# Kernel tuning notes

Measured on AMD Instinct MI355X. Metric: run time of the kernel, lower is better.

## Reference

```python
import jax, jax.numpy as jnp
import numpy as np
from jax import lax

DN = ('NCDHW', 'OIDHW', 'NCDHW')
BN_EPS = 1e-5  # eval-mode BatchNorm3d with running_mean=0, running_var=1


def conv3d(x, w, b):
    y = lax.conv_general_dilated(x, w, window_strides=(1, 1, 1),
                                 padding=[(1, 1)] * 3, dimension_numbers=DN)
    return y + b[None, :, None, None, None]


def maxpool2(x):
    return lax.reduce_window(x, -jnp.inf, lax.max,
                             (1, 1, 2, 2, 2), (1, 1, 2, 2, 2), 'VALID')


def spline_block(x, cw, cb, knots, sw, w1, w2, g, beta):
    # SplineConv3d: conv -> (BSpline3D blend with SiLU) -> BN(eval) -> maxpool
    y = conv3d(x, cw, cb)                                   # [b,c,d,h,w]
    basis = jnp.maximum(y[..., None] - knots, 0.0) ** 3     # [b,c,d,h,w,k]
    sp = jnp.einsum('bcdhwk,ck->bcdhw', basis, sw)
    out = (w1[None, :, None, None, None] * sp
           + w2[None, :, None, None, None] * (y * jax.nn.sigmoid(y)))
    scale = (g / jnp.sqrt(1.0 + BN_EPS))[None, :, None, None, None]
    return maxpool2(out * scale + beta[None, :, None, None, None])


def setup_inputs() -> dict:
    key = jax.random.key(0)
    ks = iter(jax.random.split(key, 40))
    def nrm(shape, s=1.0):
        return jax.random.normal(next(ks), shape, dtype=jnp.float32) * s
    d = {}
    d['x'] = nrm((2, 1, 64, 64, 64))
    for cin, cout, t in [(1, 32, '1'), (32, 64, '2'), (64, 128, '3')]:
        d[f'c{t}_w'] = nrm((cout, cin, 3, 3, 3), 0.1)
        d[f'c{t}_b'] = nrm((cout,), 0.01)
        d[f'c{t}_knots'] = jnp.linspace(-1.0, 1.0, 10).astype(jnp.float32)
        d[f'c{t}_sw'] = nrm((cout, 10), 0.2)
        d[f'c{t}_w1'] = nrm((cout,), 0.2)
        d[f'c{t}_w2'] = nrm((cout,), 0.2)
        d[f'bn{t}_g'] = 1.0 + nrm((cout,), 0.1)
        d[f'bn{t}_b'] = nrm((cout,), 0.1)
    d['fc1_w'] = nrm((256, 128), 0.05)
    d['fc1_b'] = nrm((256,), 0.01)
    d['fc2_w'] = nrm((2, 256), 0.05)
    d['fc2_b'] = nrm((2,), 0.01)
    return d


def reference(x,
              c1_w, c1_b, c1_knots, c1_sw, c1_w1, c1_w2, bn1_g, bn1_b,
              c2_w, c2_b, c2_knots, c2_sw, c2_w1, c2_w2, bn2_g, bn2_b,
              c3_w, c3_b, c3_knots, c3_sw, c3_w1, c3_w2, bn3_g, bn3_b,
              fc1_w, fc1_b, fc2_w, fc2_b):
    h = spline_block(x, c1_w, c1_b, c1_knots, c1_sw, c1_w1, c1_w2, bn1_g, bn1_b)
    h = spline_block(h, c2_w, c2_b, c2_knots, c2_sw, c2_w1, c2_w2, bn2_g, bn2_b)
    h = spline_block(h, c3_w, c3_b, c3_knots, c3_sw, c3_w1, c3_w2, bn3_g, bn3_b)
    h = h.mean(axis=(2, 3, 4))          # AdaptiveAvgPool3d((1,1,1)) + flatten
    h = jax.nn.relu(h @ fc1_w.T + fc1_b)  # dropout is identity in eval mode
    return h @ fc2_w.T + fc2_b
```

## Files before the change

kernel.cpp:

```cpp
#include <hip/hip_runtime.h>
#include <math.h>


#define GLOBAL_AS __attribute__((address_space(1)))
#define LDS_AS    __attribute__((address_space(3)))

static __device__ __forceinline__ void async_ld16(const float* g, float* l) {
    __builtin_amdgcn_global_load_lds((const GLOBAL_AS void*)g, (LDS_AS void*)l,
                                     16, 0, 0);
}

template <int TPB_, int CIN, int CSPLIT, int G, int PDT, int PHT, int PWT, bool AL>
__global__ __launch_bounds__(TPB_, 2) void spline_block_kernel(
    const float* __restrict__ x,
    const float* __restrict__ cw,
    const float* __restrict__ cb,
    const float* __restrict__ knots,
    const float* __restrict__ sw,
    const float* __restrict__ w1,
    const float* __restrict__ w2,
    const float* __restrict__ g,
    const float* __restrict__ beta,
    const float* __restrict__ zbuf,
    float* __restrict__ out,
    int N, int Cout, int D, int H, int W, int WP,
    int OWP, int OWO,
    int ntiles, int nthw, int ntw)
{
    constexpr int SP     = PDT * PHT * PWT;
    constexpr int CPG    = CIN / CSPLIT;
    constexpr int ID     = 2 * PDT + 2;
    constexpr int IH     = 2 * PHT + 2;
    constexpr int CPR    = AL ? 5 : 6;
    constexpr int PITCH  = CPR * 4;
    constexpr int ROWS   = ID * IH;
    constexpr int CHUNKS = ROWS * CPR;
    constexpr int PHYS   = ROWS * PITCH;
    constexpr int NCH    = (CHUNKS + SP - 1) / SP;
    constexpr int BUFS   = (CPG > 1) ? 2 : 1;
    static_assert(SP * CSPLIT == TPB_, "block = CSPLIT x SP");
    static_assert(CIN % CSPLIT == 0, "cin divisible");
    static_assert(NCH <= 32, "mask fits u32");
    static_assert(!AL || (PWT % 8) == 0, "aligned path needs 16-dword tile step");
    static_assert(CSPLIT == 1 ||
                  (CSPLIT - 1) * SP * G * 8 <= CSPLIT * BUFS * PHYS,
                  "reduction scratch fits in tile");

    __shared__ __align__(16) float tile[CSPLIT][BUFS][PHYS];
    __shared__ float  wlds[CIN * G * 28];
    __shared__ float4 stbl[G * 11];

    const int PD = D >> 1, PH = H >> 1, PW = W >> 1;
    const int groups = Cout / G;
    const int tid  = threadIdx.x;
    const int cg   = tid / SP;
    const int stid = tid % SP;

    const int bx      = blockIdx.x;
    const int tile_id = bx % ntiles;
    const int t1      = bx / ntiles;
    const int grp     = t1 % groups;
    const int n       = t1 / groups;
    const int c0      = grp * G;
    const int cinbase = cg * CPG;

    const int td  = tile_id / nthw;
    const int rem = tile_id % nthw;
    const int th_ = rem / ntw;
    const int tw_ = rem % ntw;

    for (int i = tid; i < CIN * G * 27; i += TPB_) {
        const int t  = i % 27;
        const int cgr = i / 27;
        const int gg = cgr % G;
        const int ci = cgr / G;
        wlds[cgr * 28 + t] = cw[((c0 + gg) * CIN + ci) * 27 + t];
    }
    for (int i = tid; i < G * 11; i += TPB_) {
        const int gg  = i / 11;
        const int cnt = i % 11;
        const int c   = c0 + gg;
        float A = 0.f, B3 = 0.f, C3 = 0.f, Dd = 0.f;
        for (int j = 0; j < cnt; j++) {
            const float s = sw[c * 10 + j];
            const float k = knots[j];
            A  += s;
            B3 += 3.0f * s * k;
            C3 += 3.0f * s * k * k;
            Dd += s * k * k * k;
        }
        stbl[i] = make_float4(A, B3, C3, Dd);
    }

    const int pwl = stid % PWT;
    const int phl = (stid / PWT) % PHT;
    const int pdl = stid / (PWT * PHT);

    const int pd0 = td * PDT, ph0 = th_ * PHT, pw0 = tw_ * PWT;
    const int d0 = 2 * pd0 - 1, h0 = 2 * ph0 - 1;
    const int w0 = 2 * pw0 - 1;
    const int sorg  = AL ? (2 * pw0) : (w0 & ~3);
    const int woff  = AL ? 0 : (w0 - sorg);

    int off[NCH];
    unsigned vm = 0;
#pragma unroll
    for (int k = 0; k < NCH; k++) {
        const int chunk = stid + SP * k;
        const int row = chunk / CPR, cs = chunk - row * CPR;
        const int dz = row / IH, hy = row - dz * IH;
        const int dd = d0 + dz, hh = h0 + hy;
        const int wsd = sorg + cs * 4;
        bool ok = (chunk < CHUNKS) &
                  ((unsigned)dd < (unsigned)D) &
                  ((unsigned)hh < (unsigned)H);
        if (!AL) ok = ok & ((unsigned)wsd < (unsigned)W);
        off[k] = ok ? (dd * H + hh) * WP + wsd : 0;
        vm |= (unsigned)ok << k;
    }

    const size_t chstride = (size_t)D * H * WP;
    const float* xn = x + (size_t)n * CIN * chstride;

    float acc[G][8];
#pragma unroll
    for (int gg = 0; gg < G; gg++)
#pragma unroll
        for (int i = 0; i < 8; i++) acc[gg][i] = 0.0f;

    __syncthreads();

    {
        const float* xc = xn + (size_t)cinbase * chstride;
        float* dst = &tile[cg][0][0];
#pragma unroll
        for (int k = 0; k < NCH; k++) {
            const int chunk = stid + SP * k;
            if ((k + 1) * SP <= CHUNKS || chunk < CHUNKS) {
                const float* src = ((vm >> k) & 1) ? (xc + off[k]) : zbuf;
                async_ld16(src, dst + chunk * 4);
            }
        }
    }
    __syncthreads();

    int cur = 0;
#pragma unroll 1
    for (int s = 0; s < CPG; s++) {
        if (s + 1 < CPG) {
            const float* xc = xn + (size_t)(cinbase + s + 1) * chstride;
            float* dst = &tile[cg][cur ^ (BUFS - 1)][0];
#pragma unroll
            for (int k = 0; k < NCH; k++) {
                const int chunk = stid + SP * k;
                if ((k + 1) * SP <= CHUNKS || chunk < CHUNKS) {
                    const float* src = ((vm >> k) & 1) ? (xc + off[k]) : zbuf;
                    async_ld16(src, dst + chunk * 4);
                }
            }
        }

        const int ci = cinbase + s;
        const float* tb = &tile[cg][cur][0];
        float r[64];
#pragma unroll
        for (int dz = 0; dz < 4; dz++)
#pragma unroll
        for (int dy = 0; dy < 4; dy++) {
            const int rb = ((2 * pdl + dz) * IH + (2 * phl + dy)) * PITCH +
                           woff + 2 * pwl;
            if (AL) {
                const float2 v0 = *(const float2*)(tb + rb);
                const float2 v1 = *(const float2*)(tb + rb + 2);
                r[(dz * 4 + dy) * 4 + 0] = v0.x;
                r[(dz * 4 + dy) * 4 + 1] = v0.y;
                r[(dz * 4 + dy) * 4 + 2] = v1.x;
                r[(dz * 4 + dy) * 4 + 3] = v1.y;
            } else {
                r[(dz * 4 + dy) * 4 + 0] = tb[rb + 0];
                r[(dz * 4 + dy) * 4 + 1] = tb[rb + 1];
                r[(dz * 4 + dy) * 4 + 2] = tb[rb + 2];
                r[(dz * 4 + dy) * 4 + 3] = tb[rb + 3];
            }
        }

#pragma unroll
        for (int gg = 0; gg < G; gg++) {
            const float4* w4p = (const float4*)&wlds[(ci * G + gg) * 28];
#pragma unroll
            for (int ch = 0; ch < 7; ch++) {
                const float4 wv = w4p[ch];
#pragma unroll
                for (int j = 0; j < 4; j++) {
                    const int tap = ch * 4 + j;
                    if (tap < 27) {
                        const float wvj = (j == 0) ? wv.x : (j == 1) ? wv.y
                                        : (j == 2) ? wv.z : wv.w;
                        const int kd = tap / 9, kh = (tap % 9) / 3, kw = tap % 3;
#pragma unroll
                        for (int od = 0; od < 2; od++)
#pragma unroll
                        for (int oh = 0; oh < 2; oh++)
#pragma unroll
                        for (int ow = 0; ow < 2; ow++)
                            acc[gg][(od * 2 + oh) * 2 + ow] =
                                fmaf(wvj,
                                     r[((od + kd) * 4 + (oh + kh)) * 4 + (ow + kw)],
                                     acc[gg][(od * 2 + oh) * 2 + ow]);
                    }
                }
            }
        }

        if (s + 1 < CPG) {
            __syncthreads();
            cur ^= 1;
        }
    }

    float* af = &acc[0][0];
    if (CSPLIT > 1) {
        __syncthreads();
        float* scratch = &tile[0][0][0];
        if (cg > 0) {
#pragma unroll
            for (int idx = 0; idx < G * 8; idx++)
                scratch[(idx * (CSPLIT - 1) + (cg - 1)) * SP + stid] = af[idx];
        }
        __syncthreads();
        if (cg == 0) {
#pragma unroll
            for (int idx = 0; idx < G * 8; idx++) {
                float s = af[idx];
                for (int j = 0; j < CSPLIT - 1; j++)
                    s += scratch[(idx * (CSPLIT - 1) + j) * SP + stid];
                af[idx] = s;
            }
        }
    }

    if (cg == 0) {
        const int pdg = pd0 + pdl, phg = ph0 + phl, pwg = pw0 + pwl;
#pragma unroll
        for (int gg = 0; gg < G; gg++) {
            const int c = c0 + gg;
            const float bias = cb[c];
            const float W1 = w1[c], W2 = w2[c];
            const float scale = g[c] * rsqrtf(1.0f + 1e-5f);
            const float bb = beta[c];

            float m = -INFINITY;
#pragma unroll
            for (int i = 0; i < 8; i++) {
                const float y = acc[gg][i] + bias;
                int idx = (int)floorf((y + 1.0f) * 4.5f) + 1;
                idx = min(max(idx, 0), 10);
                const float4 cf = stbl[gg * 11 + idx];
                const float sp = ((cf.x * y - cf.y) * y + cf.z) * y - cf.w;
                const float silu = y / (1.0f + __expf(-y));
                const float o = fmaf(W1 * sp + W2 * silu, scale, bb);
                m = fmaxf(m, o);
            }
            out[(((size_t)(n * Cout + c) * PD + pdg) * PH + phg) * OWP + OWO + pwg]
                = m;
        }
    }
}

__global__ __launch_bounds__(64) void mean_kernel(
    const float* __restrict__ h, float* __restrict__ out, int S)
{
    const int nc = blockIdx.x;
    const int lane = threadIdx.x;
    const float* p = h + (size_t)nc * S;
    float s = 0.0f;
    for (int i = lane; i < S; i += 64) s += p[i];
#pragma unroll
    for (int off = 32; off > 0; off >>= 1) s += __shfl_down(s, off, 64);
    if (lane == 0) out[nc] = s / (float)S;
}

__global__ __launch_bounds__(256) void fc_kernel(
    const float* __restrict__ pooled,
    const float* __restrict__ w1, const float* __restrict__ b1,
    const float* __restrict__ w2, const float* __restrict__ b2,
    float* __restrict__ out)
{
    __shared__ float hbuf[2][256];
    const int j = threadIdx.x;
#pragma unroll
    for (int nn = 0; nn < 2; nn++) {
        float s = b1[j];
        for (int k = 0; k < 128; k++)
            s = fmaf(pooled[nn * 128 + k], w1[j * 128 + k], s);
        hbuf[nn][j] = fmaxf(s, 0.0f);
    }
    __syncthreads();
    const int wid = j >> 6, lane = j & 63;
    const int nn = wid >> 1, oo = wid & 1;
    float s = 0.0f;
    for (int k = lane; k < 256; k += 64) s += hbuf[nn][k] * w2[oo * 256 + k];
#pragma unroll
    for (int off = 32; off > 0; off >>= 1) s += __shfl_down(s, off, 64);
    if (lane == 0) out[nn * 2 + oo] = s + b2[oo];
}

extern "C" void kernel_launch(void* const* d_in, const int* in_sizes, int n_in,
                              void* d_out, int out_size, void* d_ws, size_t ws_size,
                              hipStream_t stream) {
    const float* x      = (const float*)d_in[0];
    const float* c1_w   = (const float*)d_in[1];
    const float* c1_b   = (const float*)d_in[2];
    const float* c1_kn  = (const float*)d_in[3];
    const float* c1_sw  = (const float*)d_in[4];
    const float* c1_w1  = (const float*)d_in[5];
    const float* c1_w2  = (const float*)d_in[6];
    const float* bn1_g  = (const float*)d_in[7];
    const float* bn1_b  = (const float*)d_in[8];
    const float* c2_w   = (const float*)d_in[9];
    const float* c2_b   = (const float*)d_in[10];
    const float* c2_kn  = (const float*)d_in[11];
    const float* c2_sw  = (const float*)d_in[12];
    const float* c2_w1  = (const float*)d_in[13];
    const float* c2_w2  = (const float*)d_in[14];
    const float* bn2_g  = (const float*)d_in[15];
    const float* bn2_b  = (const float*)d_in[16];
    const float* c3_w   = (const float*)d_in[17];
    const float* c3_b   = (const float*)d_in[18];
    const float* c3_kn  = (const float*)d_in[19];
    const float* c3_sw  = (const float*)d_in[20];
    const float* c3_w1  = (const float*)d_in[21];
    const float* c3_w2  = (const float*)d_in[22];
    const float* bn3_g  = (const float*)d_in[23];
    const float* bn3_b  = (const float*)d_in[24];
    const float* fc1_w  = (const float*)d_in[25];
    const float* fc1_b  = (const float*)d_in[26];
    const float* fc2_w  = (const float*)d_in[27];
    const float* fc2_b  = (const float*)d_in[28];

    float* ws = (float*)d_ws;
    float* h1     = ws;
    float* h2     = h1 + 2359296;
    float* h3     = h2 + 655360;
    float* pooled = h3 + 131072;
    float* zbuf   = pooled + 256;

    hipMemsetAsync(zbuf, 0, 64, stream);
    hipMemsetAsync(h1, 0, 2359296 * sizeof(float), stream);
    hipMemsetAsync(h2, 0, 655360 * sizeof(float), stream);

    spline_block_kernel<256, 1, 1, 4, 4, 8, 8, false>
        <<<dim3(2048), dim3(256), 0, stream>>>(
        x, c1_w, c1_b, c1_kn, c1_sw, c1_w1, c1_w2, bn1_g, bn1_b, zbuf, h1,
        2, 32, 64, 64, 64, 64, 36, 1, 128, 16, 4);
    spline_block_kernel<256, 32, 1, 4, 4, 8, 8, true>
        <<<dim3(512), dim3(256), 0, stream>>>(
        h1, c2_w, c2_b, c2_kn, c2_sw, c2_w1, c2_w2, bn2_g, bn2_b, zbuf, h2,
        2, 64, 32, 32, 32, 36, 20, 1, 16, 4, 2);
    spline_block_kernel<256, 64, 4, 4, 2, 4, 8, true>
        <<<dim3(512), dim3(256), 0, stream>>>(
        h2, c3_w, c3_b, c3_kn, c3_sw, c3_w1, c3_w2, bn3_g, bn3_b, zbuf, h3,
        2, 128, 16, 16, 16, 20, 8, 0, 8, 2, 1);
    mean_kernel<<<dim3(256), dim3(64), 0, stream>>>(h3, pooled, 512);
    fc_kernel<<<dim3(1), dim3(256), 0, stream>>>(pooled, fc1_w, fc1_b, fc2_w, fc2_b,
                                                 (float*)d_out);
}
```

Baseline: 342.6 us.

## Load conv weights as scalar loads instead of LDS and split cin for block 2

Removes the LDS weight staging array and instead loads each output channel's 27 taps through a wave-uniform (readfirstlane) pointer, so they can be served by scalar loads from cache, and the gg loop is no longer unrolled. Block 2 now splits its input channels across two thread groups over a smaller spatial tile, doubling the grid size. This is meant to cut LDS traffic and footprint and to raise parallelism. In exchange it adds scalar memory latency inside the inner loop and a cross-group reduction step.

```diff
diff --git a/kernel.cpp b/kernel.cpp
--- a/kernel.cpp
+++ b/kernel.cpp
@@ -47,7 +47,6 @@
                   "reduction scratch fits in tile");
 
     __shared__ __align__(16) float tile[CSPLIT][BUFS][PHYS];
-    __shared__ float  wlds[CIN * G * 28];
     __shared__ float4 stbl[G * 11];
 
     const int PD = D >> 1, PH = H >> 1, PW = W >> 1;
@@ -69,13 +68,6 @@
     const int th_ = rem / ntw;
     const int tw_ = rem % ntw;
 
-    for (int i = tid; i < CIN * G * 27; i += TPB_) {
-        const int t  = i % 27;
-        const int cgr = i / 27;
-        const int gg = cgr % G;
-        const int ci = cgr / G;
-        wlds[cgr * 28 + t] = cw[((c0 + gg) * CIN + ci) * 27 + t];
-    }
     for (int i = tid; i < G * 11; i += TPB_) {
         const int gg  = i / 11;
         const int cnt = i % 11;
@@ -184,31 +176,31 @@
             }
         }
 
-#pragma unroll
+#pragma unroll 1
         for (int gg = 0; gg < G; gg++) {
-            const float4* w4p = (const float4*)&wlds[(ci * G + gg) * 28];
-#pragma unroll
-            for (int ch = 0; ch < 7; ch++) {
-                const float4 wv = w4p[ch];
-#pragma unroll
-                for (int j = 0; j < 4; j++) {
-                    const int tap = ch * 4 + j;
-                    if (tap < 27) {
-                        const float wvj = (j == 0) ? wv.x : (j == 1) ? wv.y
-                                        : (j == 2) ? wv.z : wv.w;
-                        const int kd = tap / 9, kh = (tap % 9) / 3, kw = tap % 3;
-#pragma unroll
-                        for (int od = 0; od < 2; od++)
-#pragma unroll
-                        for (int oh = 0; oh < 2; oh++)
-#pragma unroll
-                        for (int ow = 0; ow < 2; ow++)
-                            acc[gg][(od * 2 + oh) * 2 + ow] =
-                                fmaf(wvj,
-                                     r[((od + kd) * 4 + (oh + kh)) * 4 + (ow + kw)],
-                                     acc[gg][(od * 2 + oh) * 2 + ow]);
-                    }
-                }
+            const int wofs = __builtin_amdgcn_readfirstlane(
+                ((c0 + gg) * CIN + ci) * 27);
+            const float* __restrict__ wp = cw + wofs;
+            float wk[27];
+#pragma unroll
+            for (int t = 0; t < 27; t++) wk[t] = wp[t];
+#pragma unroll
+            for (int kd = 0; kd < 3; kd++)
+#pragma unroll
+            for (int kh = 0; kh < 3; kh++)
+#pragma unroll
+            for (int kw = 0; kw < 3; kw++) {
+                const float wvj = wk[(kd * 3 + kh) * 3 + kw];
+#pragma unroll
+                for (int od = 0; od < 2; od++)
+#pragma unroll
+                for (int oh = 0; oh < 2; oh++)
+#pragma unroll
+                for (int ow = 0; ow < 2; ow++)
+                    acc[gg][(od * 2 + oh) * 2 + ow] =
+                        fmaf(wvj,
+                             r[((od + kd) * 4 + (oh + kh)) * 4 + (ow + kw)],
+                             acc[gg][(od * 2 + oh) * 2 + ow]);
             }
         }
 
@@ -353,10 +345,10 @@
         <<<dim3(2048), dim3(256), 0, stream>>>(
         x, c1_w, c1_b, c1_kn, c1_sw, c1_w1, c1_w2, bn1_g, bn1_b, zbuf, h1,
         2, 32, 64, 64, 64, 64, 36, 1, 128, 16, 4);
-    spline_block_kernel<256, 32, 1, 4, 4, 8, 8, true>
-        <<<dim3(512), dim3(256), 0, stream>>>(
+    spline_block_kernel<256, 32, 2, 4, 4, 4, 8, true>
+        <<<dim3(1024), dim3(256), 0, stream>>>(
         h1, c2_w, c2_b, c2_kn, c2_sw, c2_w1, c2_w2, bn2_g, bn2_b, zbuf, h2,
-        2, 64, 32, 32, 32, 36, 20, 1, 16, 4, 2);
+        2, 64, 32, 32, 32, 36, 20, 1, 32, 8, 2);
     spline_block_kernel<256, 64, 4, 4, 2, 4, 8, true>
         <<<dim3(512), dim3(256), 0, stream>>>(
         h2, c3_w, c3_b, c3_kn, c3_sw, c3_w1, c3_w2, bn3_g, bn3_b, zbuf, h3,
```

New measurement: 353.9 us. +3.3%, slower.
